# Kernel tuning notes

Measured on AMD Instinct MI355X. Metric: run time of the kernel, lower is better.

## Reference

```python
import jax, jax.numpy as jnp
import numpy as np

N = 50000      # nodes
E = 1600000    # edges
R = 12         # relations (num_unique_edge_attrs)
F_IN = 64      # num_node_features
H = 128        # hidden_channels
C = 10         # num_classes
G = 256        # graphs in batch
EPS = 1e-5     # BatchNorm eps


def setup_inputs() -> dict:
    key = jax.random.key(0)
    ks = jax.random.split(key, 10)
    s = 0.05
    return {
        "x": jax.random.normal(ks[0], (N, F_IN), jnp.float32),
        "Wrel1": jax.random.normal(ks[1], (R, F_IN, H), jnp.float32) * s,
        "root1": jax.random.normal(ks[2], (F_IN, H), jnp.float32) * s,
        "bias1": jnp.zeros((H,), jnp.float32),
        "gamma1": jnp.ones((H,), jnp.float32),
        "beta1": jnp.zeros((H,), jnp.float32),
        "Wrel2": jax.random.normal(ks[3], (R, H, H), jnp.float32) * s,
        "root2": jax.random.normal(ks[4], (H, H), jnp.float32) * s,
        "bias2": jnp.zeros((H,), jnp.float32),
        "gamma2": jnp.ones((H,), jnp.float32),
        "beta2": jnp.zeros((H,), jnp.float32),
        "Wf": jax.random.normal(ks[5], (H, C), jnp.float32) * s,
        "bf": jnp.zeros((C,), jnp.float32),
        "edge_index": jax.random.randint(ks[6], (2, E), 0, N, dtype=jnp.int64) if jax.config.jax_enable_x64 else jax.random.randint(ks[6], (2, E), 0, N),
        "edge_type": jax.random.randint(ks[7], (E,), 0, R),
        "batch": jnp.sort(jax.random.randint(ks[8], (N,), 0, G)),
    }


def _segment_mean(vals, idx, num):
    # mean aggregation; empty segments -> 0
    s = jax.ops.segment_sum(vals, idx, num_segments=num)
    c = jax.ops.segment_sum(jnp.ones(idx.shape, vals.dtype), idx, num_segments=num)
    return s / jnp.clip(c, 1.0)[:, None]


def _rgcn(x, Wrel, root, bias, src, dst, edge_type):
    # PyG RGCNConv with aggr='mean': per-relation mean of source features, then W_r
    seg = dst * R + edge_type                      # fused (node, relation) segment id
    h = _segment_mean(x[src], seg, N * R)          # [N*R, in]
    h = h.reshape(N, R, x.shape[1])
    return jnp.einsum('nri,rio->no', h, Wrel) + x @ root + bias


def _bn(x, gamma, beta):
    # BatchNorm1d training-mode math (batch statistics, biased variance)
    mu = jnp.mean(x, axis=0)
    var = jnp.mean((x - mu) ** 2, axis=0)
    return gamma * (x - mu) / jnp.sqrt(var + EPS) + beta


def reference(x, Wrel1, root1, bias1, gamma1, beta1,
              Wrel2, root2, bias2, gamma2, beta2,
              Wf, bf, edge_index, edge_type, batch):
    src, dst = edge_index[0], edge_index[1]
    h = jax.nn.relu(_bn(_rgcn(x, Wrel1, root1, bias1, src, dst, edge_type), gamma1, beta1))
    h = jax.nn.relu(_bn(_rgcn(h, Wrel2, root2, bias2, src, dst, edge_type), gamma2, beta2))
    pooled = _segment_mean(h, batch, G)            # global_mean_pool -> [G, H]
    return pooled @ Wf + bf                        # [G, C]
```

## Files before the change

### kernel.cpp

```cpp
#include <hip/hip_runtime.h>

constexpr int N_NODES = 50000;
constexpr int N_EDGES = 1600000;
constexpr int NREL    = 12;
constexpr int F_INPUT = 64;
constexpr int HID     = 128;
constexpr int NCLS    = 10;
constexpr int NGRAPH  = 256;
constexpr int NSEG    = N_NODES * NREL;
constexpr float BN_EPS = 1e-5f;

constexpr int NB    = 391;
constexpr int SEGB  = 128 * NREL;
constexpr int NBLK  = 392;
constexpr int PTPB  = 1024;
constexpr int EPB   = 4096;

typedef float v4f __attribute__((ext_vector_type(4)));
typedef short s8b __attribute__((ext_vector_type(8)));

__device__ __forceinline__ unsigned f2bf(float f) {
    unsigned u = __float_as_uint(f);
    return (u + 0x7FFFu + ((u >> 16) & 1u)) >> 16;
}
__device__ __forceinline__ unsigned pack2(float a, float b) {
    return f2bf(a) | (f2bf(b) << 16);
}

constexpr int PQ0 = 64;
constexpr int PQ1 = PQ0 + 64;
constexpr int PQ2 = PQ1 + 8192;
constexpr int PQ3 = PQ2 + 13 * F_INPUT * HID;
constexpr int PQ4 = PQ3 + 13 * HID * HID;
constexpr int PQ5 = PQ4 + N_NODES * F_INPUT / 4;
constexpr int PQ6 = PQ5 + NGRAPH;
constexpr int PREP_BLOCKS = (PQ6 + 255) / 256;

__global__ void prep(const float* __restrict__ Wrel1, const float* __restrict__ root1,
                     const float* __restrict__ Wrel2, const float* __restrict__ root2,
                     const float* __restrict__ x, const int* __restrict__ batch,
                     ushort* __restrict__ Wp1, ushort* __restrict__ Wp2,
                     ushort* __restrict__ xb,
                     float* __restrict__ bn1, float* __restrict__ bn2,
                     float* __restrict__ psum, float* __restrict__ pcnt) {
    int tid = blockIdx.x * 256 + threadIdx.x;
    const uint4 z = make_uint4(0, 0, 0, 0);
    if (tid < PQ0) { reinterpret_cast<uint4*>(bn1)[tid] = z; return; }
    if (tid < PQ1) { reinterpret_cast<uint4*>(bn2)[tid - PQ0] = z; return; }
    if (tid < PQ2) { reinterpret_cast<uint4*>(psum)[tid - PQ1] = z; return; }
    if (tid < PQ3) {
        int idx = tid - PQ2;
        int r = idx >> 13, rem = idx & 8191;
        int k = rem >> 7, n = rem & 127;
        const float* W = (r < NREL) ? (Wrel1 + (size_t)r * 8192) : root1;
        float v = W[k * HID + n];
        int b = k >> 5, kk = k & 31;
        int j = (n & 7) * 16 + (n >> 3);
        Wp1[(((size_t)(r * 2 + b)) * HID + j) * 32 + kk] = (ushort)f2bf(v);
        return;
    }
    if (tid < PQ4) {
        int idx = tid - PQ3;
        int r = idx >> 14, rem = idx & 16383;
        int k = rem >> 7, n = rem & 127;
        const float* W = (r < NREL) ? (Wrel2 + (size_t)r * 16384) : root2;
        float v = W[k * HID + n];
        int b = k >> 5, kk = k & 31;
        int j = (n & 7) * 16 + (n >> 3);
        Wp2[(((size_t)(r * 4 + b)) * HID + j) * 32 + kk] = (ushort)f2bf(v);
        return;
    }
    if (tid < PQ5) {
        int i = tid - PQ4;
        float4 v = reinterpret_cast<const float4*>(x)[i];
        uint2 o;
        o.x = pack2(v.x, v.y);
        o.y = pack2(v.z, v.w);
        reinterpret_cast<uint2*>(xb)[i] = o;
        return;
    }
    if (tid < PQ6) {
        int g = tid - PQ5;
        int lo0 = 0, hi0 = N_NODES;
        while (lo0 < hi0) { int m = (lo0 + hi0) >> 1; if (batch[m] < g) lo0 = m + 1; else hi0 = m; }
        int lo1 = lo0, hi1 = N_NODES;
        while (lo1 < hi1) { int m = (lo1 + hi1) >> 1; if (batch[m] < g + 1) lo1 = m + 1; else hi1 = m; }
        pcnt[g] = (float)(lo1 - lo0);
    }
}


__global__ __launch_bounds__(PTPB)
void part_hist(const int* __restrict__ dst, int* __restrict__ histG) {
    __shared__ int h[NB];
    int t = threadIdx.x, blk = blockIdx.x;
    if (t < NB) h[t] = 0;
    __syncthreads();
    int base = blk * EPB;
#pragma unroll
    for (int it = 0; it < EPB / PTPB; ++it) {
        int e = base + it * PTPB + t;
        if (e < N_EDGES) atomicAdd(&h[dst[e] >> 7], 1);
    }
    __syncthreads();
    if (t < NB) histG[blk * NB + t] = h[t];
}

__global__ __launch_bounds__(512)
void part_scanA(const int* __restrict__ histG, int* __restrict__ cursorG,
                int* __restrict__ bucketTot) {
    __shared__ int s[512];
    int t = threadIdx.x, b = blockIdx.x;
    int v = (t < NBLK) ? histG[t * NB + b] : 0;
    s[t] = v;
    __syncthreads();
    for (int d = 1; d < 512; d <<= 1) {
        int x = (t >= d) ? s[t - d] : 0;
        __syncthreads();
        s[t] += x;
        __syncthreads();
    }
    if (t < NBLK) cursorG[t * NB + b] = s[t] - v;
    if (t == NBLK - 1) bucketTot[b] = s[t];
}

__global__ __launch_bounds__(512)
void part_scanB(const int* __restrict__ bucketTot, int* __restrict__ bucketBase) {
    __shared__ int s[512];
    int t = threadIdx.x;
    int v = (t < NB) ? bucketTot[t] : 0;
    s[t] = v;
    __syncthreads();
    for (int d = 1; d < 512; d <<= 1) {
        int x = (t >= d) ? s[t - d] : 0;
        __syncthreads();
        s[t] += x;
        __syncthreads();
    }
    if (t <= NB) bucketBase[t] = (t == 0) ? 0 : s[t - 1];
}

__global__ __launch_bounds__(PTPB)
void part_scatter(const int* __restrict__ src, const int* __restrict__ dst,
                  const int* __restrict__ et, const int* __restrict__ cursorG,
                  const int* __restrict__ bucketBase, uint* __restrict__ ebuck) {
    __shared__ int cur[NB];
    int t = threadIdx.x, blk = blockIdx.x;
    if (t < NB) cur[t] = cursorG[blk * NB + t] + bucketBase[t];
    __syncthreads();
    int base = blk * EPB;
#pragma unroll
    for (int it = 0; it < EPB / PTPB; ++it) {
        int e = base + it * PTPB + t;
        if (e < N_EDGES) {
            int d = dst[e];
            int b = d >> 7;
            int pos = atomicAdd(&cur[b], 1);
            ebuck[pos] = (uint)src[e] | ((uint)(d & 127) << 16) | ((uint)et[e] << 23);
        }
    }
}

__global__ __launch_bounds__(256)
void csr_finalize(const uint* __restrict__ ebuck, const int* __restrict__ bucketBase,
                  int* __restrict__ off, int* __restrict__ zrow, float* __restrict__ wgt) {
    __shared__ int cnt[SEGB];
    __shared__ int cur[SEGB];
    __shared__ float winv[SEGB];
    __shared__ int partial[256];
    int t = threadIdx.x, b = blockIdx.x;
    int eb0 = bucketBase[b], eb1 = bucketBase[b + 1];
#pragma unroll
    for (int i = 0; i < 6; ++i) cnt[t * 6 + i] = 0;
    __syncthreads();
    for (int e = eb0 + t; e < eb1; e += 256) {
        uint u = ebuck[e];
        int key = (int)((u >> 16) & 127) * NREL + (int)(u >> 23);
        atomicAdd(&cnt[key], 1);
    }
    __syncthreads();
    int loc[6];
    int sum = 0;
#pragma unroll
    for (int i = 0; i < 6; ++i) { loc[i] = sum; sum += cnt[t * 6 + i]; }
    partial[t] = sum;
    __syncthreads();
    for (int d = 1; d < 256; d <<= 1) {
        int v = (t >= d) ? partial[t - d] : 0;
        __syncthreads();
        partial[t] += v;
        __syncthreads();
    }
    int tbase = (t == 0) ? 0 : partial[t - 1];
    int nodeb = b * 128;
#pragma unroll
    for (int i = 0; i < 6; ++i) {
        int s = t * 6 + i;
        int gpos = eb0 + tbase + loc[i];
        cur[s] = gpos;
        int c = cnt[s];
        winv[s] = (c > 0) ? 1.0f / (float)c : 0.f;
        int node = nodeb + s / NREL;
        if (node < N_NODES) off[node * NREL + (s % NREL)] = gpos;
    }
    __syncthreads();
    for (int e = eb0 + t; e < eb1; e += 256) {
        uint u = ebuck[e];
        int rel = (int)(u >> 23);
        int key = (int)((u >> 16) & 127) * NREL + rel;
        int pos = atomicAdd(&cur[key], 1);
        zrow[pos] = rel * N_NODES + (int)(u & 0xFFFFu);
        wgt[pos] = winv[key];
    }
    if (b == 0 && t == 0) off[NSEG] = N_EDGES;
}


template <int F>
__launch_bounds__(256)
__global__ void gemm_rel(const ushort* __restrict__ xin, const ushort* __restrict__ Wp,
                         ushort* __restrict__ Z) {
    constexpr int TN  = 128;
    constexpr int FP2 = F + 8;
    constexpr int KB  = F / 32;
    constexpr int CHW = F / 4;
    constexpr int NLD = CHW / 8;
    __shared__ __align__(16) ushort A[TN * FP2];
    const int t = threadIdx.x;
    const int n0 = blockIdx.x * TN;
    const int lane = t & 63, wave = t >> 6, q = lane >> 4, l16 = lane & 15;

    {
        const int nl = t >> 2, tid4 = t & 3;
#pragma unroll
        for (int g = 0; g < 2; ++g) {
            int row = g * 64 + nl;
            int n = n0 + row;
            uint4* dstp = reinterpret_cast<uint4*>(A + row * FP2 + tid4 * CHW);
            if (n < N_NODES) {
                const uint4* srcp =
                    reinterpret_cast<const uint4*>(xin + (size_t)n * F + tid4 * CHW);
#pragma unroll
                for (int c = 0; c < NLD; ++c) dstp[c] = srcp[c];
            } else {
                uint4 zz = make_uint4(0, 0, 0, 0);
#pragma unroll
                for (int c = 0; c < NLD; ++c) dstp[c] = zz;
            }
        }
    }
    __syncthreads();

    const int rowbase = wave * 32;
    for (int rel = 0; rel < 13; ++rel) {
        v4f acc[2][8];
#pragma unroll
        for (int st = 0; st < 2; ++st)
#pragma unroll
            for (int nt = 0; nt < 8; ++nt) acc[st][nt] = (v4f){0.f, 0.f, 0.f, 0.f};
#pragma unroll
        for (int b = 0; b < KB; ++b) {
            s8b bfr[8];
            const ushort* wb = Wp + ((size_t)(rel * KB + b) * HID + l16) * 32 + q * 8;
#pragma unroll
            for (int nt = 0; nt < 8; ++nt)
                bfr[nt] = *reinterpret_cast<const s8b*>(wb + (size_t)nt * 16 * 32);
#pragma unroll
            for (int st = 0; st < 2; ++st) {
                s8b af = *reinterpret_cast<const s8b*>(
                    A + (rowbase + st * 16 + l16) * FP2 + b * 32 + q * 8);
#pragma unroll
                for (int nt = 0; nt < 8; ++nt)
                    acc[st][nt] =
                        __builtin_amdgcn_mfma_f32_16x16x32_bf16(af, bfr[nt], acc[st][nt], 0, 0, 0);
            }
        }
        ushort* zr = Z + (size_t)rel * ((size_t)N_NODES * HID);
#pragma unroll
        for (int st = 0; st < 2; ++st) {
            int rowb = n0 + rowbase + st * 16 + q * 4;
#pragma unroll
            for (int rr = 0; rr < 4; ++rr) {
                int n = rowb + rr;
                if (n < N_NODES) {
                    uint4 o;
                    o.x = pack2(acc[st][0][rr], acc[st][1][rr]);
                    o.y = pack2(acc[st][2][rr], acc[st][3][rr]);
                    o.z = pack2(acc[st][4][rr], acc[st][5][rr]);
                    o.w = pack2(acc[st][6][rr], acc[st][7][rr]);
                    *reinterpret_cast<uint4*>(zr + (size_t)n * HID + l16 * 8) = o;
                }
            }
        }
    }
}


__launch_bounds__(256)
__global__ void agg_bn(const ushort* __restrict__ Z, const int* __restrict__ off,
                       const int* __restrict__ zrow, const float* __restrict__ wgt,
                       const float* __restrict__ bias,
                       float* __restrict__ H, float* __restrict__ bn_sum,
                       float* __restrict__ bn_sq) {
    __shared__ float RED[2][4][HID];
    const int t = threadIdx.x;
    const int lane = t & 63, wave = t >> 6;
    const int n0 = blockIdx.x * 32 + wave * 8;
    const float2 bv = *reinterpret_cast<const float2*>(bias + lane * 2);
    float ps0 = 0.f, ps1 = 0.f, pq0 = 0.f, pq1 = 0.f;

    for (int i = 0; i < 8; ++i) {
        int n = n0 + i;
        if (n >= N_NODES) break;
        int e0 = off[n * NREL];
        int ee = off[n * NREL + NREL];
        uint ur = *reinterpret_cast<const uint*>(
            Z + ((size_t)12 * N_NODES + n) * HID + lane * 2);
        float a0 = __uint_as_float(ur << 16) + bv.x;
        float a1 = __uint_as_float(ur & 0xFFFF0000u) + bv.y;
        int elast = ee - 1;
        for (int e = e0; e < ee; e += 8) {
            int zr_[8];
            float w_[8];
#pragma unroll
            for (int j = 0; j < 8; ++j) {
                int ec = min(e + j, elast);
                zr_[j] = zrow[ec];
                w_[j] = (e + j < ee) ? wgt[ec] : 0.f;
            }
            uint u_[8];
#pragma unroll
            for (int j = 0; j < 8; ++j)
                u_[j] = *reinterpret_cast<const uint*>(
                    Z + (size_t)zr_[j] * HID + lane * 2);
#pragma unroll
            for (int j = 0; j < 8; ++j) {
                a0 += __uint_as_float(u_[j] << 16) * w_[j];
                a1 += __uint_as_float(u_[j] & 0xFFFF0000u) * w_[j];
            }
        }
        *reinterpret_cast<float2*>(H + (size_t)n * HID + lane * 2) = make_float2(a0, a1);
        ps0 += a0; ps1 += a1;
        pq0 += a0 * a0; pq1 += a1 * a1;
    }
    RED[0][wave][lane * 2] = ps0; RED[0][wave][lane * 2 + 1] = ps1;
    RED[1][wave][lane * 2] = pq0; RED[1][wave][lane * 2 + 1] = pq1;
    __syncthreads();
    {
        int stat = t >> 7, col = t & 127;
        float v = RED[stat][0][col] + RED[stat][1][col] +
                  RED[stat][2][col] + RED[stat][3][col];
        if (stat == 0) atomicAdd(&bn_sum[col], v);
        else           atomicAdd(&bn_sq[col], v);
    }
}


__global__ void bn_relu_bf16(const float* __restrict__ h, const float* __restrict__ bn_sum,
                             const float* __restrict__ bn_sq, const float* __restrict__ gamma,
                             const float* __restrict__ beta, ushort* __restrict__ outb) {
    __shared__ float CA[HID], CB[HID];
    int t = threadIdx.x;
    if (t < HID) {
        float mu = bn_sum[t] * (1.0f / N_NODES);
        float var = bn_sq[t] * (1.0f / N_NODES) - mu * mu;
        float a = gamma[t] / sqrtf(var + BN_EPS);
        CA[t] = a;
        CB[t] = beta[t] - a * mu;
    }
    __syncthreads();
    int i = blockIdx.x * 256 + t;
    constexpr int TOTAL = N_NODES * HID / 4;
    if (i < TOTAL) {
        int o4 = i & 31;
        float4 a = reinterpret_cast<const float4*>(CA)[o4];
        float4 b = reinterpret_cast<const float4*>(CB)[o4];
        float4 v = reinterpret_cast<const float4*>(h)[i];
        v.x = fmaxf(a.x * v.x + b.x, 0.f);
        v.y = fmaxf(a.y * v.y + b.y, 0.f);
        v.z = fmaxf(a.z * v.z + b.z, 0.f);
        v.w = fmaxf(a.w * v.w + b.w, 0.f);
        uint2 o;
        o.x = pack2(v.x, v.y);
        o.y = pack2(v.z, v.w);
        reinterpret_cast<uint2*>(outb)[i] = o;
    }
}


__global__ void pool_bnrelu(const float* __restrict__ h, const float* __restrict__ bn_sum,
                            const float* __restrict__ bn_sq, const float* __restrict__ gamma,
                            const float* __restrict__ beta, const int* __restrict__ batch,
                            float* __restrict__ psum) {
    __shared__ float CA[HID], CB[HID];
    int t = threadIdx.x;
    if (t < HID) {
        float mu = bn_sum[t] * (1.0f / N_NODES);
        float var = bn_sq[t] * (1.0f / N_NODES) - mu * mu;
        float a = gamma[t] / sqrtf(var + BN_EPS);
        CA[t] = a;
        CB[t] = beta[t] - a * mu;
    }
    __syncthreads();
    int col = t & 127;
    int nb = blockIdx.x * 16 + (t >> 7) * 8;
    float a = CA[col], b = CB[col];
    float run = 0.f;
    int curg = -1;
    for (int i = 0; i < 8; ++i) {
        int n = nb + i;
        if (n < N_NODES) {
            int g = batch[n];
            float v = fmaxf(a * h[(size_t)n * HID + col] + b, 0.f);
            if (g != curg) {
                if (curg >= 0) atomicAdd(&psum[curg * HID + col], run);
                run = 0.f;
                curg = g;
            }
            run += v;
        }
    }
    if (curg >= 0) atomicAdd(&psum[curg * HID + col], run);
}

__global__ void final_kernel(const float* __restrict__ psum, const float* __restrict__ pcnt,
                             const float* __restrict__ Wf, const float* __restrict__ bf,
                             float* __restrict__ out) {
    __shared__ float p[HID];
    int g = blockIdx.x, t = threadIdx.x;
    float inv = 1.0f / fmaxf(pcnt[g], 1.0f);
    p[t] = psum[g * HID + t] * inv;
    p[t + 64] = psum[g * HID + t + 64] * inv;
    __syncthreads();
    if (t < NCLS) {
        float s = bf[t];
#pragma unroll 16
        for (int k = 0; k < HID; ++k) s += p[k] * Wf[k * NCLS + t];
        out[g * NCLS + t] = s;
    }
}


extern "C" void kernel_launch(void* const* d_in, const int* in_sizes, int n_in,
                              void* d_out, int out_size, void* d_ws, size_t ws_size,
                              hipStream_t stream) {
    const float* x      = (const float*)d_in[0];
    const float* Wrel1  = (const float*)d_in[1];
    const float* root1  = (const float*)d_in[2];
    const float* bias1  = (const float*)d_in[3];
    const float* gamma1 = (const float*)d_in[4];
    const float* beta1  = (const float*)d_in[5];
    const float* Wrel2  = (const float*)d_in[6];
    const float* root2  = (const float*)d_in[7];
    const float* bias2  = (const float*)d_in[8];
    const float* gamma2 = (const float*)d_in[9];
    const float* beta2  = (const float*)d_in[10];
    const float* Wf     = (const float*)d_in[11];
    const float* bf     = (const float*)d_in[12];
    const int* ei       = (const int*)d_in[13];
    const int* et       = (const int*)d_in[14];
    const int* batch    = (const int*)d_in[15];
    const int* srcv = ei;
    const int* dstv = ei + N_EDGES;

    char* w = (char*)d_ws;
    auto alloc = [&](size_t bytes) -> char* {
        char* p = w;
        w += (bytes + 255) / 256 * 256;
        return p;
    };
    int* off     = (int*)alloc((size_t)(NSEG + 1) * 4);
    int* zrow    = (int*)alloc((size_t)N_EDGES * 4);
    float* wgt   = (float*)alloc((size_t)N_EDGES * 4);
    ushort* xb   = (ushort*)alloc((size_t)N_NODES * F_INPUT * 2);
    ushort* H1b  = (ushort*)alloc((size_t)N_NODES * HID * 2);
    ushort* Wp1  = (ushort*)alloc((size_t)13 * F_INPUT * HID * 2);
    ushort* Wp2  = (ushort*)alloc((size_t)13 * HID * HID * 2);
    float* bn1   = (float*)alloc(2 * HID * 4);
    float* bn2   = (float*)alloc(2 * HID * 4);
    float* psum  = (float*)alloc((size_t)NGRAPH * HID * 4);
    float* pcnt  = (float*)alloc((size_t)NGRAPH * 4);
    float* Hbuf  = (float*)alloc((size_t)N_NODES * HID * 4);
    char* ovl    = alloc((size_t)13 * N_NODES * HID * 2);
    int* histG      = (int*)ovl;
    int* cursorG    = (int*)(ovl + (size_t)NBLK * NB * 4);
    int* bucketTot  = (int*)(ovl + (size_t)2 * NBLK * NB * 4);
    int* bucketBase = (int*)(ovl + (size_t)2 * NBLK * NB * 4 + (NB + 1) * 4 + 252);
    uint* ebuck     = (uint*)(ovl + (size_t)2 * NBLK * NB * 4 + 4096);
    ushort* Zb      = (ushort*)ovl;

    prep<<<PREP_BLOCKS, 256, 0, stream>>>(Wrel1, root1, Wrel2, root2, x, batch,
                                          Wp1, Wp2, xb, bn1, bn2, psum, pcnt);

    part_hist<<<NBLK, PTPB, 0, stream>>>(dstv, histG);
    part_scanA<<<NB, 512, 0, stream>>>(histG, cursorG, bucketTot);
    part_scanB<<<1, 512, 0, stream>>>(bucketTot, bucketBase);
    part_scatter<<<NBLK, PTPB, 0, stream>>>(srcv, dstv, et, cursorG, bucketBase, ebuck);
    csr_finalize<<<NB, 256, 0, stream>>>(ebuck, bucketBase, off, zrow, wgt);

    int gblk = (N_NODES + 127) / 128;
    int ablk = (N_NODES + 31) / 32;

    gemm_rel<F_INPUT><<<gblk, 256, 0, stream>>>(xb, Wp1, Zb);
    agg_bn<<<ablk, 256, 0, stream>>>(Zb, off, zrow, wgt, bias1, Hbuf, bn1, bn1 + HID);
    bn_relu_bf16<<<(N_NODES * HID / 4 + 255) / 256, 256, 0, stream>>>(Hbuf, bn1, bn1 + HID,
                                                                      gamma1, beta1, H1b);

    gemm_rel<HID><<<gblk, 256, 0, stream>>>(H1b, Wp2, Zb);
    agg_bn<<<ablk, 256, 0, stream>>>(Zb, off, zrow, wgt, bias2, Hbuf, bn2, bn2 + HID);

    pool_bnrelu<<<(N_NODES + 15) / 16, 256, 0, stream>>>(Hbuf, bn2, bn2 + HID, gamma2, beta2,
                                                         batch, psum);
    final_kernel<<<NGRAPH, 64, 0, stream>>>(psum, pcnt, Wf, bf, (float*)d_out);
}
```

Baseline: 492.8 us.

## Aggregate per-relation means before the relation GEMM instead of after

Reorders the RGCN computation so the per-(node, relation) neighbor means are gathered from the narrow input features first. A single concatenated GEMM then runs over the 12 relation means plus the root term, with bias and BatchNorm statistics fused into its epilogue and double-buffered LDS loads. This drops the per-edge weight array and the 13x hidden-width Z intermediate, and gathers 64- or 128-wide bf16 rows instead of 128-wide Z rows. In exchange it writes a 12xNxF mean buffer, adds an extra bf16 rounding of the means, and gathers with only 4-way unrolled, lane-per-feature loads.

```diff
diff --git a/kernel.cpp b/kernel.cpp
--- a/kernel.cpp
+++ b/kernel.cpp
@@ -26,6 +26,8 @@
 __device__ __forceinline__ unsigned pack2(float a, float b) {
     return f2bf(a) | (f2bf(b) << 16);
 }
+__device__ __forceinline__ float bflo(unsigned u) { return __uint_as_float(u << 16); }
+__device__ __forceinline__ float bfhi(unsigned u) { return __uint_as_float(u & 0xFFFF0000u); }
 
 constexpr int PQ0 = 64;
 constexpr int PQ1 = PQ0 + 64;
@@ -163,10 +165,9 @@
 
 __global__ __launch_bounds__(256)
 void csr_finalize(const uint* __restrict__ ebuck, const int* __restrict__ bucketBase,
-                  int* __restrict__ off, int* __restrict__ zrow, float* __restrict__ wgt) {
+                  int* __restrict__ off, int* __restrict__ zrow) {
     __shared__ int cnt[SEGB];
     __shared__ int cur[SEGB];
-    __shared__ float winv[SEGB];
     __shared__ int partial[256];
     int t = threadIdx.x, b = blockIdx.x;
     int eb0 = bucketBase[b], eb1 = bucketBase[b + 1];
@@ -198,66 +199,122 @@
         int s = t * 6 + i;
         int gpos = eb0 + tbase + loc[i];
         cur[s] = gpos;
-        int c = cnt[s];
-        winv[s] = (c > 0) ? 1.0f / (float)c : 0.f;
         int node = nodeb + s / NREL;
         if (node < N_NODES) off[node * NREL + (s % NREL)] = gpos;
     }
     __syncthreads();
     for (int e = eb0 + t; e < eb1; e += 256) {
         uint u = ebuck[e];
-        int rel = (int)(u >> 23);
-        int key = (int)((u >> 16) & 127) * NREL + rel;
+        int key = (int)((u >> 16) & 127) * NREL + (int)(u >> 23);
         int pos = atomicAdd(&cur[key], 1);
-        zrow[pos] = rel * N_NODES + (int)(u & 0xFFFFu);
-        wgt[pos] = winv[key];
+        zrow[pos] = (int)(u & 0xFFFFu);
     }
     if (b == 0 && t == 0) off[NSEG] = N_EDGES;
 }
 
 
 template <int F>
-__launch_bounds__(256)
-__global__ void gemm_rel(const ushort* __restrict__ xin, const ushort* __restrict__ Wp,
-                         ushort* __restrict__ Z) {
+__global__ __launch_bounds__(256)
+void agg_mean(const ushort* __restrict__ X, const int* __restrict__ off,
+              const int* __restrict__ zrow, ushort* __restrict__ M) {
+    const int n = blockIdx.x * 4 + (threadIdx.x >> 6);
+    if (n >= N_NODES) return;
+    const int lane = threadIdx.x & 63;
+    const int* offn = off + n * NREL;
+    int e0 = offn[0];
+#pragma unroll
+    for (int rel = 0; rel < NREL; ++rel) {
+        int e1 = offn[rel + 1];
+        float a0 = 0.f, a1 = 0.f;
+        for (int e = e0; e < e1; e += 4) {
+            const int rem = e1 - e;
+            uint u0 = 0, u1 = 0, u2 = 0, u3 = 0;
+            if constexpr (F == 64) {
+                u0 = X[(size_t)zrow[e] * 64 + lane];
+                if (rem > 1) u1 = X[(size_t)zrow[e + 1] * 64 + lane];
+                if (rem > 2) u2 = X[(size_t)zrow[e + 2] * 64 + lane];
+                if (rem > 3) u3 = X[(size_t)zrow[e + 3] * 64 + lane];
+                a0 += bflo(u0) + bflo(u1) + bflo(u2) + bflo(u3);
+            } else {
+                u0 = *reinterpret_cast<const uint*>(X + (size_t)zrow[e] * 128 + lane * 2);
+                if (rem > 1) u1 = *reinterpret_cast<const uint*>(X + (size_t)zrow[e + 1] * 128 + lane * 2);
+                if (rem > 2) u2 = *reinterpret_cast<const uint*>(X + (size_t)zrow[e + 2] * 128 + lane * 2);
+                if (rem > 3) u3 = *reinterpret_cast<const uint*>(X + (size_t)zrow[e + 3] * 128 + lane * 2);
+                a0 += bflo(u0) + bflo(u1) + bflo(u2) + bflo(u3);
+                a1 += bfhi(u0) + bfhi(u1) + bfhi(u2) + bfhi(u3);
+            }
+        }
+        int cnt = e1 - e0;
+        float winv = (cnt > 0) ? 1.f / (float)cnt : 0.f;
+        ushort* mrow = M + ((size_t)rel * N_NODES + n) * F;
+        if constexpr (F == 64) {
+            mrow[lane] = (ushort)f2bf(a0 * winv);
+        } else {
+            *reinterpret_cast<uint*>(mrow + lane * 2) = pack2(a0 * winv, a1 * winv);
+        }
+        e0 = e1;
+    }
+}
+
+
+template <int F>
+__global__ __launch_bounds__(256)
+void gemm_cat(const ushort* __restrict__ M, const ushort* __restrict__ xin,
+              const ushort* __restrict__ Wp, const float* __restrict__ bias,
+              float* __restrict__ H, float* __restrict__ bn_sum,
+              float* __restrict__ bn_sq) {
     constexpr int TN  = 128;
     constexpr int FP2 = F + 8;
     constexpr int KB  = F / 32;
     constexpr int CHW = F / 4;
     constexpr int NLD = CHW / 8;
-    __shared__ __align__(16) ushort A[TN * FP2];
+    __shared__ __align__(16) ushort A[2][TN * FP2];
+    __shared__ float BNred[2][4][HID];
     const int t = threadIdx.x;
     const int n0 = blockIdx.x * TN;
     const int lane = t & 63, wave = t >> 6, q = lane >> 4, l16 = lane & 15;
-
-    {
-        const int nl = t >> 2, tid4 = t & 3;
+    const int nl = t >> 2, tid4 = t & 3;
+
+    uint4 st_reg[2][NLD];
+    auto ldrel = [&](int rel) {
+        const ushort* base = (rel < NREL) ? (M + (size_t)rel * N_NODES * F) : xin;
 #pragma unroll
         for (int g = 0; g < 2; ++g) {
-            int row = g * 64 + nl;
-            int n = n0 + row;
-            uint4* dstp = reinterpret_cast<uint4*>(A + row * FP2 + tid4 * CHW);
+            int n = n0 + g * 64 + nl;
             if (n < N_NODES) {
-                const uint4* srcp =
-                    reinterpret_cast<const uint4*>(xin + (size_t)n * F + tid4 * CHW);
-#pragma unroll
-                for (int c = 0; c < NLD; ++c) dstp[c] = srcp[c];
+                const uint4* sp =
+                    reinterpret_cast<const uint4*>(base + (size_t)n * F + tid4 * CHW);
+#pragma unroll
+                for (int c = 0; c < NLD; ++c) st_reg[g][c] = sp[c];
             } else {
                 uint4 zz = make_uint4(0, 0, 0, 0);
 #pragma unroll
-                for (int c = 0; c < NLD; ++c) dstp[c] = zz;
+                for (int c = 0; c < NLD; ++c) st_reg[g][c] = zz;
             }
         }
-    }
-    __syncthreads();
-
-    const int rowbase = wave * 32;
+    };
+    auto wrrel = [&](int buf) {
+#pragma unroll
+        for (int g = 0; g < 2; ++g) {
+            uint4* dp = reinterpret_cast<uint4*>(A[buf] + (g * 64 + nl) * FP2 + tid4 * CHW);
+#pragma unroll
+            for (int c = 0; c < NLD; ++c) dp[c] = st_reg[g][c];
+        }
+    };
+
+    ldrel(0);
+    wrrel(0);
+
+    v4f acc[2][8];
+#pragma unroll
+    for (int st = 0; st < 2; ++st)
+#pragma unroll
+        for (int nt = 0; nt < 8; ++nt) acc[st][nt] = (v4f){0.f, 0.f, 0.f, 0.f};
+
+    int cur = 0;
     for (int rel = 0; rel < 13; ++rel) {
-        v4f acc[2][8];
-#pragma unroll
-        for (int st = 0; st < 2; ++st)
-#pragma unroll
-            for (int nt = 0; nt < 8; ++nt) acc[st][nt] = (v4f){0.f, 0.f, 0.f, 0.f};
+        if (rel < 12) ldrel(rel + 1);
+        __syncthreads();
 #pragma unroll
         for (int b = 0; b < KB; ++b) {
             s8b bfr[8];
@@ -268,90 +325,60 @@
 #pragma unroll
             for (int st = 0; st < 2; ++st) {
                 s8b af = *reinterpret_cast<const s8b*>(
-                    A + (rowbase + st * 16 + l16) * FP2 + b * 32 + q * 8);
+                    A[cur] + (wave * 32 + st * 16 + l16) * FP2 + b * 32 + q * 8);
 #pragma unroll
                 for (int nt = 0; nt < 8; ++nt)
                     acc[st][nt] =
                         __builtin_amdgcn_mfma_f32_16x16x32_bf16(af, bfr[nt], acc[st][nt], 0, 0, 0);
             }
         }
-        ushort* zr = Z + (size_t)rel * ((size_t)N_NODES * HID);
-#pragma unroll
-        for (int st = 0; st < 2; ++st) {
-            int rowb = n0 + rowbase + st * 16 + q * 4;
-#pragma unroll
-            for (int rr = 0; rr < 4; ++rr) {
-                int n = rowb + rr;
-                if (n < N_NODES) {
-                    uint4 o;
-                    o.x = pack2(acc[st][0][rr], acc[st][1][rr]);
-                    o.y = pack2(acc[st][2][rr], acc[st][3][rr]);
-                    o.z = pack2(acc[st][4][rr], acc[st][5][rr]);
-                    o.w = pack2(acc[st][6][rr], acc[st][7][rr]);
-                    *reinterpret_cast<uint4*>(zr + (size_t)n * HID + l16 * 8) = o;
+        if (rel < 12) { wrrel(cur ^ 1); cur ^= 1; }
+    }
+
+    const int c0 = l16 * 8;
+    float4 b4a = *reinterpret_cast<const float4*>(bias + c0);
+    float4 b4b = *reinterpret_cast<const float4*>(bias + c0 + 4);
+    float bv[8] = {b4a.x, b4a.y, b4a.z, b4a.w, b4b.x, b4b.y, b4b.z, b4b.w};
+    float s[8], sq[8];
+#pragma unroll
+    for (int nt = 0; nt < 8; ++nt) { s[nt] = 0.f; sq[nt] = 0.f; }
+#pragma unroll
+    for (int st = 0; st < 2; ++st) {
+#pragma unroll
+        for (int rr = 0; rr < 4; ++rr) {
+            int n = n0 + wave * 32 + st * 16 + q * 4 + rr;
+            if (n < N_NODES) {
+                float v[8];
+#pragma unroll
+                for (int nt = 0; nt < 8; ++nt) {
+                    v[nt] = acc[st][nt][rr] + bv[nt];
+                    s[nt] += v[nt];
+                    sq[nt] += v[nt] * v[nt];
                 }
+                float* hr = H + (size_t)n * HID + c0;
+                *reinterpret_cast<float4*>(hr)     = make_float4(v[0], v[1], v[2], v[3]);
+                *reinterpret_cast<float4*>(hr + 4) = make_float4(v[4], v[5], v[6], v[7]);
             }
         }
     }
-}
-
-
-__launch_bounds__(256)
-__global__ void agg_bn(const ushort* __restrict__ Z, const int* __restrict__ off,
-                       const int* __restrict__ zrow, const float* __restrict__ wgt,
-                       const float* __restrict__ bias,
-                       float* __restrict__ H, float* __restrict__ bn_sum,
-                       float* __restrict__ bn_sq) {
-    __shared__ float RED[2][4][HID];
-    const int t = threadIdx.x;
-    const int lane = t & 63, wave = t >> 6;
-    const int n0 = blockIdx.x * 32 + wave * 8;
-    const float2 bv = *reinterpret_cast<const float2*>(bias + lane * 2);
-    float ps0 = 0.f, ps1 = 0.f, pq0 = 0.f, pq1 = 0.f;
-
-    for (int i = 0; i < 8; ++i) {
-        int n = n0 + i;
-        if (n >= N_NODES) break;
-        int e0 = off[n * NREL];
-        int ee = off[n * NREL + NREL];
-        uint ur = *reinterpret_cast<const uint*>(
-            Z + ((size_t)12 * N_NODES + n) * HID + lane * 2);
-        float a0 = __uint_as_float(ur << 16) + bv.x;
-        float a1 = __uint_as_float(ur & 0xFFFF0000u) + bv.y;
-        int elast = ee - 1;
-        for (int e = e0; e < ee; e += 8) {
-            int zr_[8];
-            float w_[8];
-#pragma unroll
-            for (int j = 0; j < 8; ++j) {
-                int ec = min(e + j, elast);
-                zr_[j] = zrow[ec];
-                w_[j] = (e + j < ee) ? wgt[ec] : 0.f;
-            }
-            uint u_[8];
-#pragma unroll
-            for (int j = 0; j < 8; ++j)
-                u_[j] = *reinterpret_cast<const uint*>(
-                    Z + (size_t)zr_[j] * HID + lane * 2);
-#pragma unroll
-            for (int j = 0; j < 8; ++j) {
-                a0 += __uint_as_float(u_[j] << 16) * w_[j];
-                a1 += __uint_as_float(u_[j] & 0xFFFF0000u) * w_[j];
-            }
-        }
-        *reinterpret_cast<float2*>(H + (size_t)n * HID + lane * 2) = make_float2(a0, a1);
-        ps0 += a0; ps1 += a1;
-        pq0 += a0 * a0; pq1 += a1 * a1;
-    }
-    RED[0][wave][lane * 2] = ps0; RED[0][wave][lane * 2 + 1] = ps1;
-    RED[1][wave][lane * 2] = pq0; RED[1][wave][lane * 2 + 1] = pq1;
-    __syncthreads();
-    {
-        int stat = t >> 7, col = t & 127;
-        float v = RED[stat][0][col] + RED[stat][1][col] +
-                  RED[stat][2][col] + RED[stat][3][col];
-        if (stat == 0) atomicAdd(&bn_sum[col], v);
-        else           atomicAdd(&bn_sq[col], v);
+#pragma unroll
+    for (int nt = 0; nt < 8; ++nt) {
+        s[nt]  += __shfl_xor(s[nt], 16);  s[nt]  += __shfl_xor(s[nt], 32);
+        sq[nt] += __shfl_xor(sq[nt], 16); sq[nt] += __shfl_xor(sq[nt], 32);
+    }
+    if (q == 0) {
+#pragma unroll
+        for (int nt = 0; nt < 8; ++nt) {
+            BNred[0][wave][c0 + nt] = s[nt];
+            BNred[1][wave][c0 + nt] = sq[nt];
+        }
+    }
+    __syncthreads();
+    if (t < HID) {
+        atomicAdd(&bn_sum[t], BNred[0][0][t] + BNred[0][1][t] + BNred[0][2][t] + BNred[0][3][t]);
+    } else {
+        int c = t - HID;
+        atomicAdd(&bn_sq[c], BNred[1][0][c] + BNred[1][1][c] + BNred[1][2][c] + BNred[1][3][c]);
     }
 }
 
@@ -471,7 +498,6 @@
     };
     int* off     = (int*)alloc((size_t)(NSEG + 1) * 4);
     int* zrow    = (int*)alloc((size_t)N_EDGES * 4);
-    float* wgt   = (float*)alloc((size_t)N_EDGES * 4);
     ushort* xb   = (ushort*)alloc((size_t)N_NODES * F_INPUT * 2);
     ushort* H1b  = (ushort*)alloc((size_t)N_NODES * HID * 2);
     ushort* Wp1  = (ushort*)alloc((size_t)13 * F_INPUT * HID * 2);
@@ -481,13 +507,13 @@
     float* psum  = (float*)alloc((size_t)NGRAPH * HID * 4);
     float* pcnt  = (float*)alloc((size_t)NGRAPH * 4);
     float* Hbuf  = (float*)alloc((size_t)N_NODES * HID * 4);
-    char* ovl    = alloc((size_t)13 * N_NODES * HID * 2);
+    char* ovl    = alloc((size_t)12 * N_NODES * HID * 2);
     int* histG      = (int*)ovl;
     int* cursorG    = (int*)(ovl + (size_t)NBLK * NB * 4);
     int* bucketTot  = (int*)(ovl + (size_t)2 * NBLK * NB * 4);
     int* bucketBase = (int*)(ovl + (size_t)2 * NBLK * NB * 4 + (NB + 1) * 4 + 252);
     uint* ebuck     = (uint*)(ovl + (size_t)2 * NBLK * NB * 4 + 4096);
-    ushort* Zb      = (ushort*)ovl;
+    ushort* Mb      = (ushort*)ovl;
 
     prep<<<PREP_BLOCKS, 256, 0, stream>>>(Wrel1, root1, Wrel2, root2, x, batch,
                                           Wp1, Wp2, xb, bn1, bn2, psum, pcnt);
@@ -496,18 +522,18 @@
     part_scanA<<<NB, 512, 0, stream>>>(histG, cursorG, bucketTot);
     part_scanB<<<1, 512, 0, stream>>>(bucketTot, bucketBase);
     part_scatter<<<NBLK, PTPB, 0, stream>>>(srcv, dstv, et, cursorG, bucketBase, ebuck);
-    csr_finalize<<<NB, 256, 0, stream>>>(ebuck, bucketBase, off, zrow, wgt);
+    csr_finalize<<<NB, 256, 0, stream>>>(ebuck, bucketBase, off, zrow);
 
     int gblk = (N_NODES + 127) / 128;
-    int ablk = (N_NODES + 31) / 32;
-
-    gemm_rel<F_INPUT><<<gblk, 256, 0, stream>>>(xb, Wp1, Zb);
-    agg_bn<<<ablk, 256, 0, stream>>>(Zb, off, zrow, wgt, bias1, Hbuf, bn1, bn1 + HID);
+    int mblk = (N_NODES + 3) / 4;
+
+    agg_mean<F_INPUT><<<mblk, 256, 0, stream>>>(xb, off, zrow, Mb);
+    gemm_cat<F_INPUT><<<gblk, 256, 0, stream>>>(Mb, xb, Wp1, bias1, Hbuf, bn1, bn1 + HID);
     bn_relu_bf16<<<(N_NODES * HID / 4 + 255) / 256, 256, 0, stream>>>(Hbuf, bn1, bn1 + HID,
                                                                       gamma1, beta1, H1b);
 
-    gemm_rel<HID><<<gblk, 256, 0, stream>>>(H1b, Wp2, Zb);
-    agg_bn<<<ablk, 256, 0, stream>>>(Zb, off, zrow, wgt, bias2, Hbuf, bn2, bn2 + HID);
+    agg_mean<HID><<<mblk, 256, 0, stream>>>(H1b, off, zrow, Mb);
+    gemm_cat<HID><<<gblk, 256, 0, stream>>>(Mb, H1b, Wp2, bias2, Hbuf, bn2, bn2 + HID);
 
     pool_bnrelu<<<(N_NODES + 15) / 16, 256, 0, stream>>>(Hbuf, bn2, bn2 + HID, gamma2, beta2,
                                                          batch, psum);
```

Result: slower. 583.8 us (+18.5%).
